# Kernel tuning notes

Measured on AMD Instinct MI355X. Metric: run time of the kernel, lower is better.

Reference implementation:

```python
import jax, jax.numpy as jnp
import numpy as np
import math

N_SLOTS, DIM, ITERS = 8, 256, 3
BATCH, TOKENS = 64, 4096


def _ln(x, g, b, eps=1e-5):
    mu = x.mean(-1, keepdims=True)
    var = ((x - mu) ** 2).mean(-1, keepdims=True)
    return (x - mu) * jax.lax.rsqrt(var + eps) * g + b


def setup_inputs() -> dict:
    key = jax.random.key(0)
    ks = jax.random.split(key, 16)
    d = DIM
    s = 0.02
    return {
        "inputs": jax.random.normal(ks[0], (BATCH, TOKENS, d), jnp.float32),
        "noise": jax.random.normal(ks[1], (BATCH, N_SLOTS, d), jnp.float32),
        "slots_mu": jax.random.normal(ks[2], (1, N_SLOTS, d), jnp.float32),
        "slots_logsigma": jnp.zeros((1, N_SLOTS, d), jnp.float32),
        "Wq": jax.random.normal(ks[3], (d, d), jnp.float32) * s,
        "Wk": jax.random.normal(ks[4], (d, d), jnp.float32) * s,
        "Wv": jax.random.normal(ks[5], (d, d), jnp.float32) * s,
        "W_ih": jax.random.normal(ks[6], (3 * d, d), jnp.float32) * s,
        "W_hh": jax.random.normal(ks[7], (3 * d, d), jnp.float32) * s,
        "b_ih": jnp.zeros((3 * d,), jnp.float32),
        "b_hh": jnp.zeros((3 * d,), jnp.float32),
        "mlp_W1": jax.random.normal(ks[8], (d, d), jnp.float32) * s,
        "mlp_b1": jnp.zeros((d,), jnp.float32),
        "mlp_W2": jax.random.normal(ks[9], (d, d), jnp.float32) * s,
        "mlp_b2": jnp.zeros((d,), jnp.float32),
        "ln_in_g": jnp.ones((d,), jnp.float32),
        "ln_in_b": jnp.zeros((d,), jnp.float32),
        "ln_slots_g": jnp.ones((d,), jnp.float32),
        "ln_slots_b": jnp.zeros((d,), jnp.float32),
        "ln_mlp_g": jnp.ones((d,), jnp.float32),
        "ln_mlp_b": jnp.zeros((d,), jnp.float32),
    }


def reference(inputs, noise, slots_mu, slots_logsigma, Wq, Wk, Wv,
              W_ih, W_hh, b_ih, b_hh, mlp_W1, mlp_b1, mlp_W2, mlp_b2,
              ln_in_g, ln_in_b, ln_slots_g, ln_slots_b, ln_mlp_g, ln_mlp_b):
    n, t, d = inputs.shape
    scale = 1.0 / math.sqrt(d)
    x = _ln(inputs, ln_in_g, ln_in_b)                      # [n,t,d]
    slots = slots_mu + jnp.exp(slots_logsigma) * noise     # [n,S,d]
    k = jnp.einsum('ntd,ed->nte', x, Wk)
    v = jnp.einsum('ntd,ed->nte', x, Wv)
    for _ in range(ITERS):
        slots_prev = slots
        q = jnp.einsum('nsd,ed->nse', _ln(slots, ln_slots_g, ln_slots_b), Wq)
        logits = jnp.einsum('nsd,ntd->nst', q, k) * scale  # [n,S,t]
        attn = jax.nn.softmax(logits, axis=-1)
        attn = attn / (attn.sum(-1, keepdims=True) + 1e-8)
        updates = jnp.einsum('nst,ntd->nsd', attn, v)      # [n,S,d]
        # GRUCell (torch gate order r,z,n)
        gi = jnp.einsum('nsd,ed->nse', updates, W_ih) + b_ih
        gh = jnp.einsum('nsd,ed->nse', slots_prev, W_hh) + b_hh
        gi_r, gi_z, gi_n = jnp.split(gi, 3, axis=-1)
        gh_r, gh_z, gh_n = jnp.split(gh, 3, axis=-1)
        r = jax.nn.sigmoid(gi_r + gh_r)
        z = jax.nn.sigmoid(gi_z + gh_z)
        h_new = jnp.tanh(gi_n + r * gh_n)
        slots = (1.0 - z) * h_new + z * slots_prev
        hid = jax.nn.relu(jnp.einsum('nsd,ed->nse', _ln(slots, ln_mlp_g, ln_mlp_b), mlp_W1) + mlp_b1)
        slots = slots + jnp.einsum('nsd,ed->nse', hid, mlp_W2) + mlp_b2
    return slots
```

## Files before the change

### kernel.cpp

```cpp
#include <hip/hip_runtime.h>
#include <math.h>

#define TOKENS 4096
#define BATCH 64

typedef __attribute__((ext_vector_type(8))) short bf16x8;
typedef __attribute__((ext_vector_type(4))) float f32x4;
union U4B { uint4 u; bf16x8 b; };
union U2x2B { uint2 u[2]; bf16x8 b; };

__device__ __forceinline__ float wsum(float v) {
#pragma unroll
  for (int m = 32; m >= 1; m >>= 1) v += __shfl_xor(v, m);
  return v;
}
__device__ __forceinline__ unsigned short f2bf(float f) {
  unsigned u = __float_as_uint(f);
  u += 0x7fffu + ((u >> 16) & 1u);
  return (unsigned short)(u >> 16);
}
__device__ __forceinline__ float bflo(unsigned p) { return __uint_as_float(p << 16); }
__device__ __forceinline__ float bfhi(unsigned p) { return __uint_as_float(p & 0xffff0000u); }
__device__ __forceinline__ float sigmf(float x) { return 1.f / (1.f + expf(-x)); }

__global__ __launch_bounds__(256) void k_pre(
    const float* __restrict__ in, const float* __restrict__ lin_g,
    const float* __restrict__ lin_b, unsigned* __restrict__ x,
    const float* __restrict__ Wq, const float* __restrict__ Wv,
    const float* __restrict__ Wih, const float* __restrict__ Whh,
    const float* __restrict__ W1, const float* __restrict__ W2,
    float* __restrict__ WqT, float* __restrict__ WvT, float* __restrict__ WihT,
    float* __restrict__ WhhT, float* __restrict__ W1T, float* __restrict__ W2T) {
  int bid = blockIdx.x, tid = threadIdx.x;
  if (bid < 65536) {
    int row = bid * 4 + (tid >> 6);
    int lane = tid & 63;
    const float* p = in + (size_t)row * 256 + lane * 4;
    float4 v = *(const float4*)p;
    float s  = wsum(v.x + v.y + v.z + v.w);
    float sq = wsum(v.x * v.x + v.y * v.y + v.z * v.z + v.w * v.w);
    float mu = s * (1.f / 256.f);
    float var = sq * (1.f / 256.f) - mu * mu;
    float rs = rsqrtf(var + 1e-5f);
    float4 gg = *(const float4*)(lin_g + lane * 4);
    float4 bb = *(const float4*)(lin_b + lane * 4);
    float y0 = (v.x - mu) * rs * gg.x + bb.x;
    float y1 = (v.y - mu) * rs * gg.y + bb.y;
    float y2 = (v.z - mu) * rs * gg.z + bb.z;
    float y3 = (v.w - mu) * rs * gg.w + bb.w;
    uint2 o;
    o.x = (unsigned)f2bf(y0) | ((unsigned)f2bf(y1) << 16);
    o.y = (unsigned)f2bf(y2) | ((unsigned)f2bf(y3) << 16);
    *(uint2*)(x + (size_t)row * 128 + lane * 2) = o;
    return;
  }
  {
    __shared__ float t[32][33];
    int t2 = bid - 65536;
    const float* S; float* D; int R; int tile;
    if (t2 < 64)       { S = Wq;  D = WqT;  R = 256; tile = t2; }
    else if (t2 < 128) { S = Wv;  D = WvT;  R = 256; tile = t2 - 64; }
    else if (t2 < 192) { S = W1;  D = W1T;  R = 256; tile = t2 - 128; }
    else if (t2 < 256) { S = W2;  D = W2T;  R = 256; tile = t2 - 192; }
    else if (t2 < 448) { S = Wih; D = WihT; R = 768; tile = t2 - 256; }
    else               { S = Whh; D = WhhT; R = 768; tile = t2 - 448; }
    int rt = R >> 5;
    int r0 = (tile % rt) * 32, c0 = (tile / rt) * 32;
    int ci = tid & 31, r8 = tid >> 5;
#pragma unroll
    for (int k = 0; k < 4; ++k) {
      int r = r8 + k * 8;
      t[r][ci] = S[(size_t)(r0 + r) * 256 + c0 + ci];
    }
    __syncthreads();
#pragma unroll
    for (int k = 0; k < 4; ++k) {
      int r = r8 + k * 8;
      D[(size_t)(c0 + r) * R + r0 + ci] = t[ci][r];
    }
  }
}

__global__ __launch_bounds__(256) void k_qw0(
    const float* __restrict__ smu, const float* __restrict__ slsig,
    const float* __restrict__ noise, const float* __restrict__ lsl_g,
    const float* __restrict__ lsl_b, const float* __restrict__ WqT,
    const float* __restrict__ Wk, float* __restrict__ slots,
    unsigned* __restrict__ qwb) {
  __shared__ float ln[256];
  __shared__ float q[256];
  __shared__ float red[8];
  int n = blockIdx.x, s = blockIdx.y, tid = threadIdx.x;
  int sd = s * 256 + tid;
  float v = smu[sd] + expf(slsig[sd]) * noise[(size_t)n * 2048 + sd];
  slots[(size_t)n * 2048 + sd] = v;
  float ps = wsum(v), pq = wsum(v * v);
  if ((tid & 63) == 0) { red[tid >> 6] = ps; red[4 + (tid >> 6)] = pq; }
  __syncthreads();
  float sum = red[0] + red[1] + red[2] + red[3];
  float sqq = red[4] + red[5] + red[6] + red[7];
  float mu = sum * (1.f / 256.f);
  float var = sqq * (1.f / 256.f) - mu * mu;
  float rs = rsqrtf(var + 1e-5f);
  ln[tid] = (v - mu) * rs * lsl_g[tid] + lsl_b[tid];
  __syncthreads();
  float a = 0.f;
  for (int d = 0; d < 256; ++d) a += ln[d] * WqT[d * 256 + tid];
  q[tid] = a;
  __syncthreads();
  float c = 0.f;
  for (int e = 0; e < 256; ++e) c += q[e] * Wk[(size_t)e * 256 + tid];
  c *= 0.0625f;
  __syncthreads();
  ln[tid] = c;
  __syncthreads();
  if (tid < 128)
    qwb[((size_t)n * 8 + s) * 128 + tid] =
        (unsigned)f2bf(ln[2 * tid]) | ((unsigned)f2bf(ln[2 * tid + 1]) << 16);
}

__global__ __launch_bounds__(256) void k_att(const unsigned* __restrict__ x,
                                             const unsigned* __restrict__ qwb,
                                             float* __restrict__ stats,
                                             float* __restrict__ axp) {
  __shared__ unsigned xs[64][130];
  __shared__ float lsT[64][8];
  __shared__ float redS[8][4];
  int ch = blockIdx.x, n = blockIdx.y;
  int tid = threadIdx.x, wv = tid >> 6, l = tid & 63;
  int col = l & 15, g = l >> 4;
  {
    int lane32 = tid & 31, g8 = tid >> 5;
    const unsigned* src = x + ((size_t)n * 4096 + ch * 64) * 128 + lane32 * 4;
#pragma unroll
    for (int p = 0; p < 8; ++p) {
      int row = p * 8 + g8;
      uint4 vv = *(const uint4*)(src + (size_t)row * 128);
      unsigned* dr = &xs[row][lane32 * 4];
      *(uint2*)dr = make_uint2(vv.x, vv.y);
      *(uint2*)(dr + 2) = make_uint2(vv.z, vv.w);
    }
  }
  uint4 a[8];
  {
    const unsigned* ap = qwb + ((size_t)n * 8 + (l & 7)) * 128 + g * 4;
#pragma unroll
    for (int kk = 0; kk < 8; ++kk) a[kk] = *(const uint4*)(ap + kk * 16);
  }
  __syncthreads();
  {
    int t0 = wv * 16;
    const unsigned* xr = &xs[t0 + col][0];
    f32x4 qacc = {0.f, 0.f, 0.f, 0.f};
#pragma unroll
    for (int kk = 0; kk < 8; ++kk) {
      U4B aa; aa.u = a[kk];
      U2x2B bb;
      bb.u[0] = *(const uint2*)(xr + kk * 16 + g * 4);
      bb.u[1] = *(const uint2*)(xr + kk * 16 + g * 4 + 2);
      qacc = __builtin_amdgcn_mfma_f32_16x16x32_bf16(aa.b, bb.b, qacc, 0, 0, 0);
    }
    if (g < 2) {
#pragma unroll
      for (int r = 0; r < 4; ++r) lsT[t0 + col][g * 4 + r] = qacc[r];
    }
  }
  __syncthreads();
  int s = tid & 7, tg = tid >> 3;
  {
    float e0 = __expf(lsT[tg][s]);
    float e1 = __expf(lsT[tg + 32][s]);
    lsT[tg][s] = e0;
    lsT[tg + 32][s] = e1;
    float S = e0 + e1;
    S += __shfl_xor(S, 8);
    S += __shfl_xor(S, 16);
    S += __shfl_xor(S, 32);
    if (l < 8) redS[s][wv] = S;
  }
  __syncthreads();
  if (tid < 8)
    stats[((size_t)n * 8 + tid) * 64 + ch] =
        redS[tid][0] + redS[tid][1] + redS[tid][2] + redS[tid][3];
  {
    int d = tid;
    float pv[8] = {0, 0, 0, 0, 0, 0, 0, 0};
#pragma unroll 8
    for (int t = 0; t < 64; ++t) {
      unsigned pw = xs[t][d >> 1];
      float xv = (d & 1) ? bfhi(pw) : bflo(pw);
      float4 p0 = *(const float4*)&lsT[t][0];
      float4 p1 = *(const float4*)&lsT[t][4];
      pv[0] += p0.x * xv; pv[1] += p0.y * xv;
      pv[2] += p0.z * xv; pv[3] += p0.w * xv;
      pv[4] += p1.x * xv; pv[5] += p1.y * xv;
      pv[6] += p1.z * xv; pv[7] += p1.w * xv;
    }
    float* op = axp + ((size_t)n * 64 + ch) * 2048 + d;
#pragma unroll
    for (int ss = 0; ss < 8; ++ss) op[ss * 256] = pv[ss];
  }
}

__global__ __launch_bounds__(512) void k_update3(
    const float* __restrict__ axp, const float* __restrict__ stats,
    const float* __restrict__ slots_in,
    const float* __restrict__ WvT, const float* __restrict__ WihT,
    const float* __restrict__ WhhT, const float* __restrict__ b_ih,
    const float* __restrict__ b_hh, const float* __restrict__ W1T,
    const float* __restrict__ b1, const float* __restrict__ W2T,
    const float* __restrict__ b2, const float* __restrict__ lml_g,
    const float* __restrict__ lml_b, const float* __restrict__ lsl_g,
    const float* __restrict__ lsl_b, const float* __restrict__ WqT,
    const float* __restrict__ Wk, unsigned* __restrict__ qwb, int doQw,
    float* __restrict__ slots_out) {
  __shared__ float ax[4][256];
  __shared__ float sp[4][256];
  __shared__ float upd[4][256];
  __shared__ float gi[4][768];
  __shared__ float gh[4][768];
  __shared__ float sn[4][256];
  __shared__ float lnv[4][256];
  __shared__ float hid[4][256];
  __shared__ float red[16];
  __shared__ float Sinv[4];
  int n = blockIdx.x, sg = blockIdx.y * 4;
  int tid = threadIdx.x;
  if (tid < 4) {
    const float* st = stats + ((size_t)n * 8 + sg + tid) * 64;
    float S = 0.f;
#pragma unroll 8
    for (int c = 0; c < 64; ++c) S += st[c];
    Sinv[tid] = 1.f / (S * (1.f + 1e-8f));
  }
  __syncthreads();
  for (int i = tid; i < 1024; i += 512) {
    int sl = i >> 8, d = i & 255;
    const float* pp = axp + (size_t)n * 131072 + (sg + sl) * 256 + d;
    float a = 0.f;
#pragma unroll 8
    for (int c = 0; c < 64; ++c) a += pp[(size_t)c * 2048];
    ax[sl][d] = a * Sinv[sl];
    sp[sl][d] = slots_in[((size_t)n * 8 + sg + sl) * 256 + d];
  }
  __syncthreads();
  int e = tid & 255, h = tid >> 8;
  {
    float a0 = 0.f, a1 = 0.f;
    for (int d = 0; d < 256; ++d) {
      float w = WvT[d * 256 + e];
      a0 += ax[h * 2][d] * w;
      a1 += ax[h * 2 + 1][d] * w;
    }
    upd[h * 2][e] = a0;
    upd[h * 2 + 1][e] = a1;
  }
  __syncthreads();
  for (int jj = tid; jj < 1536; jj += 512) {
    bool ihs = jj < 768;
    int j = ihs ? jj : jj - 768;
    const float* WT = ihs ? WihT : WhhT;
    const float* src = ihs ? &upd[0][0] : &sp[0][0];
    float a0 = 0.f, a1 = 0.f, a2 = 0.f, a3 = 0.f;
    for (int d = 0; d < 256; ++d) {
      float w = WT[(size_t)d * 768 + j];
      a0 += src[d] * w;
      a1 += src[256 + d] * w;
      a2 += src[512 + d] * w;
      a3 += src[768 + d] * w;
    }
    float bb = ihs ? b_ih[j] : b_hh[j];
    float* dst = ihs ? &gi[0][0] : &gh[0][0];
    dst[j] = a0 + bb;
    dst[768 + j] = a1 + bb;
    dst[1536 + j] = a2 + bb;
    dst[2304 + j] = a3 + bb;
  }
  __syncthreads();
  for (int i = tid; i < 1024; i += 512) {
    int sl = i >> 8, j = i & 255;
    float r = sigmf(gi[sl][j] + gh[sl][j]);
    float z = sigmf(gi[sl][j + 256] + gh[sl][j + 256]);
    float hh = tanhf(gi[sl][j + 512] + r * gh[sl][j + 512]);
    sn[sl][j] = (1.f - z) * hh + z * sp[sl][j];
  }
  __syncthreads();
  {
    int sl = tid >> 7, qq = tid & 127;
    float v0 = sn[sl][qq], v1 = sn[sl][qq + 128];
    float ps = wsum(v0 + v1);
    float pq = wsum(v0 * v0 + v1 * v1);
    int wid = tid >> 6;
    if ((tid & 63) == 0) { red[wid] = ps; red[8 + wid] = pq; }
    __syncthreads();
    float ssum = red[sl * 2] + red[sl * 2 + 1];
    float sqq  = red[8 + sl * 2] + red[8 + sl * 2 + 1];
    float mu = ssum * (1.f / 256.f);
    float var = sqq * (1.f / 256.f) - mu * mu;
    float rs = rsqrtf(var + 1e-5f);
    lnv[sl][qq]       = (v0 - mu) * rs * lml_g[qq] + lml_b[qq];
    lnv[sl][qq + 128] = (v1 - mu) * rs * lml_g[qq + 128] + lml_b[qq + 128];
  }
  __syncthreads();
  {
    float a0 = 0.f, a1 = 0.f;
    for (int d = 0; d < 256; ++d) {
      float w = W1T[d * 256 + e];
      a0 += lnv[h * 2][d] * w;
      a1 += lnv[h * 2 + 1][d] * w;
    }
    hid[h * 2][e]     = fmaxf(a0 + b1[e], 0.f);
    hid[h * 2 + 1][e] = fmaxf(a1 + b1[e], 0.f);
  }
  __syncthreads();
  {
    float a0 = 0.f, a1 = 0.f;
    for (int d = 0; d < 256; ++d) {
      float w = W2T[d * 256 + e];
      a0 += hid[h * 2][d] * w;
      a1 += hid[h * 2 + 1][d] * w;
    }
    float o0 = sn[h * 2][e] + a0 + b2[e];
    float o1 = sn[h * 2 + 1][e] + a1 + b2[e];
    slots_out[((size_t)n * 8 + sg + h * 2) * 256 + e]     = o0;
    slots_out[((size_t)n * 8 + sg + h * 2 + 1) * 256 + e] = o1;
    ax[h * 2][e] = o0;
    ax[h * 2 + 1][e] = o1;
  }
  if (!doQw) return;
  __syncthreads();
  {
    int sl = tid >> 7, qq = tid & 127;
    float v0 = ax[sl][qq], v1 = ax[sl][qq + 128];
    float ps = wsum(v0 + v1);
    float pq = wsum(v0 * v0 + v1 * v1);
    int wid = tid >> 6;
    if ((tid & 63) == 0) { red[wid] = ps; red[8 + wid] = pq; }
    __syncthreads();
    float ssum = red[sl * 2] + red[sl * 2 + 1];
    float sqq  = red[8 + sl * 2] + red[8 + sl * 2 + 1];
    float mu = ssum * (1.f / 256.f);
    float var = sqq * (1.f / 256.f) - mu * mu;
    float rs = rsqrtf(var + 1e-5f);
    sp[sl][qq]       = (v0 - mu) * rs * lsl_g[qq] + lsl_b[qq];
    sp[sl][qq + 128] = (v1 - mu) * rs * lsl_g[qq + 128] + lsl_b[qq + 128];
  }
  __syncthreads();
  {
    float a0 = 0.f, a1 = 0.f;
    for (int d = 0; d < 256; ++d) {
      float w = WqT[d * 256 + e];
      a0 += sp[h * 2][d] * w;
      a1 += sp[h * 2 + 1][d] * w;
    }
    upd[h * 2][e] = a0;
    upd[h * 2 + 1][e] = a1;
  }
  __syncthreads();
  {
    float c0 = 0.f, c1 = 0.f;
    for (int ee = 0; ee < 256; ++ee) {
      float w = Wk[(size_t)ee * 256 + e];
      c0 += upd[h * 2][ee] * w;
      c1 += upd[h * 2 + 1][ee] * w;
    }
    hid[h * 2][e]     = c0 * 0.0625f;
    hid[h * 2 + 1][e] = c1 * 0.0625f;
  }
  __syncthreads();
  {
    int sl = tid >> 7, p = tid & 127;
    qwb[((size_t)n * 8 + sg + sl) * 128 + p] =
        (unsigned)f2bf(hid[sl][2 * p]) | ((unsigned)f2bf(hid[sl][2 * p + 1]) << 16);
  }
}

extern "C" void kernel_launch(void* const* d_in, const int* in_sizes, int n_in,
                              void* d_out, int out_size, void* d_ws, size_t ws_size,
                              hipStream_t stream) {
  (void)in_sizes; (void)n_in; (void)out_size; (void)ws_size;
  const float* inputs = (const float*)d_in[0];
  const float* noise  = (const float*)d_in[1];
  const float* smu    = (const float*)d_in[2];
  const float* slsig  = (const float*)d_in[3];
  const float* Wq     = (const float*)d_in[4];
  const float* Wk     = (const float*)d_in[5];
  const float* Wv     = (const float*)d_in[6];
  const float* W_ih   = (const float*)d_in[7];
  const float* W_hh   = (const float*)d_in[8];
  const float* b_ih   = (const float*)d_in[9];
  const float* b_hh   = (const float*)d_in[10];
  const float* W1     = (const float*)d_in[11];
  const float* b1     = (const float*)d_in[12];
  const float* W2     = (const float*)d_in[13];
  const float* b2     = (const float*)d_in[14];
  const float* lin_g  = (const float*)d_in[15];
  const float* lin_b  = (const float*)d_in[16];
  const float* lsl_g  = (const float*)d_in[17];
  const float* lsl_b  = (const float*)d_in[18];
  const float* lml_g  = (const float*)d_in[19];
  const float* lml_b  = (const float*)d_in[20];
  float* out = (float*)d_out;
  char* ws = (char*)d_ws;
  unsigned* x    = (unsigned*)(ws + 0);
  unsigned* qwb  = (unsigned*)(ws + 134217728);
  float* stats   = (float*)(ws + 134479872);
  float* axp     = (float*)(ws + 134610944);
  float* WqT     = (float*)(ws + 168165376);
  float* WvT     = (float*)(ws + 168427520);
  float* WihT    = (float*)(ws + 168689664);
  float* WhhT    = (float*)(ws + 169476096);
  float* W1T     = (float*)(ws + 170262528);
  float* W2T     = (float*)(ws + 170524672);

  k_pre<<<dim3(66176), 256, 0, stream>>>(inputs, lin_g, lin_b, x,
                                         Wq, Wv, W_ih, W_hh, W1, W2,
                                         WqT, WvT, WihT, WhhT, W1T, W2T);
  k_qw0<<<dim3(BATCH, 8), 256, 0, stream>>>(smu, slsig, noise, lsl_g, lsl_b,
                                            WqT, Wk, out, qwb);
  for (int it = 0; it < 3; ++it) {
    k_att<<<dim3(64, BATCH), 256, 0, stream>>>(x, qwb, stats, axp);
    k_update3<<<dim3(BATCH, 2), 512, 0, stream>>>(
        axp, stats, out, WvT, WihT, WhhT, b_ih, b_hh, W1T, b1, W2T, b2,
        lml_g, lml_b, lsl_g, lsl_b, WqT, Wk, qwb, (it < 2) ? 1 : 0, out);
  }
}
```

Baseline: 460.8 us.

## Process two token chunks per attention block and split update kernel per slot

The attention kernel now loops over two 64-token chunks per block, accumulating the weighted-value partials and softmax sums in registers. This halves the number of partial sums written to and later reduced from global memory. The update kernel changes from 128 blocks of 512 threads handling 4 slots each to 512 blocks of 256 threads handling one slot, with the GRU gate computation fused into the matvec loop. That gives more parallel blocks for the small serial per-slot work, at the cost of rereading the weights once per slot instead of once per four slots.

```diff
diff --git a/kernel.cpp b/kernel.cpp
--- a/kernel.cpp
+++ b/kernel.cpp
@@ -119,90 +119,97 @@
         (unsigned)f2bf(ln[2 * tid]) | ((unsigned)f2bf(ln[2 * tid + 1]) << 16);
 }
 
-__global__ __launch_bounds__(256) void k_att(const unsigned* __restrict__ x,
-                                             const unsigned* __restrict__ qwb,
-                                             float* __restrict__ stats,
-                                             float* __restrict__ axp) {
+__global__ __launch_bounds__(256) void k_att2(const unsigned* __restrict__ x,
+                                              const unsigned* __restrict__ qwb,
+                                              float* __restrict__ stats,
+                                              float* __restrict__ axp) {
   __shared__ unsigned xs[64][130];
   __shared__ float lsT[64][8];
   __shared__ float redS[8][4];
-  int ch = blockIdx.x, n = blockIdx.y;
+  int bx = blockIdx.x, n = blockIdx.y;
   int tid = threadIdx.x, wv = tid >> 6, l = tid & 63;
   int col = l & 15, g = l >> 4;
-  {
-    int lane32 = tid & 31, g8 = tid >> 5;
-    const unsigned* src = x + ((size_t)n * 4096 + ch * 64) * 128 + lane32 * 4;
-#pragma unroll
-    for (int p = 0; p < 8; ++p) {
-      int row = p * 8 + g8;
-      uint4 vv = *(const uint4*)(src + (size_t)row * 128);
-      unsigned* dr = &xs[row][lane32 * 4];
-      *(uint2*)dr = make_uint2(vv.x, vv.y);
-      *(uint2*)(dr + 2) = make_uint2(vv.z, vv.w);
-    }
-  }
   uint4 a[8];
   {
     const unsigned* ap = qwb + ((size_t)n * 8 + (l & 7)) * 128 + g * 4;
 #pragma unroll
     for (int kk = 0; kk < 8; ++kk) a[kk] = *(const uint4*)(ap + kk * 16);
   }
-  __syncthreads();
-  {
-    int t0 = wv * 16;
-    const unsigned* xr = &xs[t0 + col][0];
-    f32x4 qacc = {0.f, 0.f, 0.f, 0.f};
-#pragma unroll
-    for (int kk = 0; kk < 8; ++kk) {
-      U4B aa; aa.u = a[kk];
-      U2x2B bb;
-      bb.u[0] = *(const uint2*)(xr + kk * 16 + g * 4);
-      bb.u[1] = *(const uint2*)(xr + kk * 16 + g * 4 + 2);
-      qacc = __builtin_amdgcn_mfma_f32_16x16x32_bf16(aa.b, bb.b, qacc, 0, 0, 0);
-    }
-    if (g < 2) {
-#pragma unroll
-      for (int r = 0; r < 4; ++r) lsT[t0 + col][g * 4 + r] = qacc[r];
-    }
-  }
-  __syncthreads();
+  float pv[8] = {0, 0, 0, 0, 0, 0, 0, 0};
+  float SS = 0.f;
   int s = tid & 7, tg = tid >> 3;
-  {
-    float e0 = __expf(lsT[tg][s]);
-    float e1 = __expf(lsT[tg + 32][s]);
-    lsT[tg][s] = e0;
-    lsT[tg + 32][s] = e1;
-    float S = e0 + e1;
-    S += __shfl_xor(S, 8);
-    S += __shfl_xor(S, 16);
-    S += __shfl_xor(S, 32);
-    if (l < 8) redS[s][wv] = S;
-  }
-  __syncthreads();
-  if (tid < 8)
-    stats[((size_t)n * 8 + tid) * 64 + ch] =
-        redS[tid][0] + redS[tid][1] + redS[tid][2] + redS[tid][3];
-  {
-    int d = tid;
-    float pv[8] = {0, 0, 0, 0, 0, 0, 0, 0};
+  for (int cc = 0; cc < 2; ++cc) {
+    int ch = bx * 2 + cc;
+    {
+      int lane32 = tid & 31, g8 = tid >> 5;
+      const unsigned* src = x + ((size_t)n * 4096 + ch * 64) * 128 + lane32 * 4;
+#pragma unroll
+      for (int p = 0; p < 8; ++p) {
+        int row = p * 8 + g8;
+        uint4 vv = *(const uint4*)(src + (size_t)row * 128);
+        unsigned* dr = &xs[row][lane32 * 4];
+        *(uint2*)dr = make_uint2(vv.x, vv.y);
+        *(uint2*)(dr + 2) = make_uint2(vv.z, vv.w);
+      }
+    }
+    __syncthreads();
+    {
+      int t0 = wv * 16;
+      const unsigned* xr = &xs[t0 + col][0];
+      f32x4 qacc = {0.f, 0.f, 0.f, 0.f};
+#pragma unroll
+      for (int kk = 0; kk < 8; ++kk) {
+        U4B aa; aa.u = a[kk];
+        U2x2B bb;
+        bb.u[0] = *(const uint2*)(xr + kk * 16 + g * 4);
+        bb.u[1] = *(const uint2*)(xr + kk * 16 + g * 4 + 2);
+        qacc = __builtin_amdgcn_mfma_f32_16x16x32_bf16(aa.b, bb.b, qacc, 0, 0, 0);
+      }
+      if (g < 2) {
+#pragma unroll
+        for (int r = 0; r < 4; ++r) lsT[t0 + col][g * 4 + r] = qacc[r];
+      }
+    }
+    __syncthreads();
+    {
+      float e0 = __expf(lsT[tg][s]);
+      float e1 = __expf(lsT[tg + 32][s]);
+      lsT[tg][s] = e0;
+      lsT[tg + 32][s] = e1;
+      float S = e0 + e1;
+      S += __shfl_xor(S, 8);
+      S += __shfl_xor(S, 16);
+      S += __shfl_xor(S, 32);
+      if (l < 8) redS[s][wv] = S;
+    }
+    __syncthreads();
+    if (tid < 8)
+      SS += redS[tid][0] + redS[tid][1] + redS[tid][2] + redS[tid][3];
+    {
+      int d = tid;
 #pragma unroll 8
-    for (int t = 0; t < 64; ++t) {
-      unsigned pw = xs[t][d >> 1];
-      float xv = (d & 1) ? bfhi(pw) : bflo(pw);
-      float4 p0 = *(const float4*)&lsT[t][0];
-      float4 p1 = *(const float4*)&lsT[t][4];
-      pv[0] += p0.x * xv; pv[1] += p0.y * xv;
-      pv[2] += p0.z * xv; pv[3] += p0.w * xv;
-      pv[4] += p1.x * xv; pv[5] += p1.y * xv;
-      pv[6] += p1.z * xv; pv[7] += p1.w * xv;
-    }
-    float* op = axp + ((size_t)n * 64 + ch) * 2048 + d;
+      for (int t = 0; t < 64; ++t) {
+        unsigned pw = xs[t][d >> 1];
+        float xv = (d & 1) ? bfhi(pw) : bflo(pw);
+        float4 p0 = *(const float4*)&lsT[t][0];
+        float4 p1 = *(const float4*)&lsT[t][4];
+        pv[0] += p0.x * xv; pv[1] += p0.y * xv;
+        pv[2] += p0.z * xv; pv[3] += p0.w * xv;
+        pv[4] += p1.x * xv; pv[5] += p1.y * xv;
+        pv[6] += p1.z * xv; pv[7] += p1.w * xv;
+      }
+    }
+    __syncthreads();
+  }
+  if (tid < 8) stats[((size_t)n * 8 + tid) * 32 + bx] = SS;
+  {
+    float* op = axp + ((size_t)n * 32 + bx) * 2048 + tid;
 #pragma unroll
     for (int ss = 0; ss < 8; ++ss) op[ss * 256] = pv[ss];
   }
 }
 
-__global__ __launch_bounds__(512) void k_update3(
+__global__ __launch_bounds__(256) void k_update5(
     const float* __restrict__ axp, const float* __restrict__ stats,
     const float* __restrict__ slots_in,
     const float* __restrict__ WvT, const float* __restrict__ WihT,
@@ -214,165 +221,112 @@
     const float* __restrict__ lsl_b, const float* __restrict__ WqT,
     const float* __restrict__ Wk, unsigned* __restrict__ qwb, int doQw,
     float* __restrict__ slots_out) {
-  __shared__ float ax[4][256];
-  __shared__ float sp[4][256];
-  __shared__ float upd[4][256];
-  __shared__ float gi[4][768];
-  __shared__ float gh[4][768];
-  __shared__ float sn[4][256];
-  __shared__ float lnv[4][256];
-  __shared__ float hid[4][256];
-  __shared__ float red[16];
-  __shared__ float Sinv[4];
-  int n = blockIdx.x, sg = blockIdx.y * 4;
-  int tid = threadIdx.x;
-  if (tid < 4) {
-    const float* st = stats + ((size_t)n * 8 + sg + tid) * 64;
-    float S = 0.f;
+  __shared__ float ax[256];
+  __shared__ float sp[256];
+  __shared__ float upd[256];
+  __shared__ float sn[256];
+  __shared__ float lnv[256];
+  __shared__ float hid[256];
+  __shared__ float red[8];
+  int n = blockIdx.x, s = blockIdx.y, tid = threadIdx.x;
+  {
+    float sv = 0.f;
+    if (tid < 32) sv = stats[((size_t)n * 8 + s) * 32 + tid];
+    if (tid < 64) {
+      sv = wsum(sv);
+      if (tid == 0) red[0] = 1.f / (sv * (1.f + 1e-8f));
+    }
+  }
+  {
+    const float* pp = axp + (size_t)n * 65536 + s * 256 + tid;
+    float acc = 0.f;
 #pragma unroll 8
-    for (int c = 0; c < 64; ++c) S += st[c];
-    Sinv[tid] = 1.f / (S * (1.f + 1e-8f));
-  }
-  __syncthreads();
-  for (int i = tid; i < 1024; i += 512) {
-    int sl = i >> 8, d = i & 255;
-    const float* pp = axp + (size_t)n * 131072 + (sg + sl) * 256 + d;
-    float a = 0.f;
-#pragma unroll 8
-    for (int c = 0; c < 64; ++c) a += pp[(size_t)c * 2048];
-    ax[sl][d] = a * Sinv[sl];
-    sp[sl][d] = slots_in[((size_t)n * 8 + sg + sl) * 256 + d];
-  }
-  __syncthreads();
-  int e = tid & 255, h = tid >> 8;
-  {
-    float a0 = 0.f, a1 = 0.f;
+    for (int c = 0; c < 32; ++c) acc += pp[(size_t)c * 2048];
+    sp[tid] = slots_in[((size_t)n * 8 + s) * 256 + tid];
+    __syncthreads();
+    ax[tid] = acc * red[0];
+  }
+  __syncthreads();
+  {
+    float a0 = 0.f;
+    for (int d = 0; d < 256; ++d) a0 += ax[d] * WvT[d * 256 + tid];
+    upd[tid] = a0;
+  }
+  __syncthreads();
+  {
+    int j = tid;
+    float gr = 0.f, gz = 0.f, gn = 0.f, hr = 0.f, hz = 0.f, hn = 0.f;
     for (int d = 0; d < 256; ++d) {
-      float w = WvT[d * 256 + e];
-      a0 += ax[h * 2][d] * w;
-      a1 += ax[h * 2 + 1][d] * w;
-    }
-    upd[h * 2][e] = a0;
-    upd[h * 2 + 1][e] = a1;
-  }
-  __syncthreads();
-  for (int jj = tid; jj < 1536; jj += 512) {
-    bool ihs = jj < 768;
-    int j = ihs ? jj : jj - 768;
-    const float* WT = ihs ? WihT : WhhT;
-    const float* src = ihs ? &upd[0][0] : &sp[0][0];
-    float a0 = 0.f, a1 = 0.f, a2 = 0.f, a3 = 0.f;
-    for (int d = 0; d < 256; ++d) {
-      float w = WT[(size_t)d * 768 + j];
-      a0 += src[d] * w;
-      a1 += src[256 + d] * w;
-      a2 += src[512 + d] * w;
-      a3 += src[768 + d] * w;
-    }
-    float bb = ihs ? b_ih[j] : b_hh[j];
-    float* dst = ihs ? &gi[0][0] : &gh[0][0];
-    dst[j] = a0 + bb;
-    dst[768 + j] = a1 + bb;
-    dst[1536 + j] = a2 + bb;
-    dst[2304 + j] = a3 + bb;
-  }
-  __syncthreads();
-  for (int i = tid; i < 1024; i += 512) {
-    int sl = i >> 8, j = i & 255;
-    float r = sigmf(gi[sl][j] + gh[sl][j]);
-    float z = sigmf(gi[sl][j + 256] + gh[sl][j + 256]);
-    float hh = tanhf(gi[sl][j + 512] + r * gh[sl][j + 512]);
-    sn[sl][j] = (1.f - z) * hh + z * sp[sl][j];
-  }
-  __syncthreads();
-  {
-    int sl = tid >> 7, qq = tid & 127;
-    float v0 = sn[sl][qq], v1 = sn[sl][qq + 128];
-    float ps = wsum(v0 + v1);
-    float pq = wsum(v0 * v0 + v1 * v1);
-    int wid = tid >> 6;
-    if ((tid & 63) == 0) { red[wid] = ps; red[8 + wid] = pq; }
-    __syncthreads();
-    float ssum = red[sl * 2] + red[sl * 2 + 1];
-    float sqq  = red[8 + sl * 2] + red[8 + sl * 2 + 1];
-    float mu = ssum * (1.f / 256.f);
+      float u = upd[d], s_ = sp[d];
+      gr += u * WihT[d * 768 + j];
+      gz += u * WihT[d * 768 + j + 256];
+      gn += u * WihT[d * 768 + j + 512];
+      hr += s_ * WhhT[d * 768 + j];
+      hz += s_ * WhhT[d * 768 + j + 256];
+      hn += s_ * WhhT[d * 768 + j + 512];
+    }
+    float r = sigmf(gr + b_ih[j] + hr + b_hh[j]);
+    float z = sigmf(gz + b_ih[j + 256] + hz + b_hh[j + 256]);
+    float hh = tanhf(gn + b_ih[j + 512] + r * (hn + b_hh[j + 512]));
+    sn[j] = (1.f - z) * hh + z * sp[j];
+  }
+  __syncthreads();
+  {
+    float v = sn[tid];
+    float ps = wsum(v), pq = wsum(v * v);
+    if ((tid & 63) == 0) { red[tid >> 6] = ps; red[4 + (tid >> 6)] = pq; }
+    __syncthreads();
+    float sum = red[0] + red[1] + red[2] + red[3];
+    float sqq = red[4] + red[5] + red[6] + red[7];
+    float mu = sum * (1.f / 256.f);
     float var = sqq * (1.f / 256.f) - mu * mu;
     float rs = rsqrtf(var + 1e-5f);
-    lnv[sl][qq]       = (v0 - mu) * rs * lml_g[qq] + lml_b[qq];
-    lnv[sl][qq + 128] = (v1 - mu) * rs * lml_g[qq + 128] + lml_b[qq + 128];
-  }
-  __syncthreads();
-  {
-    float a0 = 0.f, a1 = 0.f;
-    for (int d = 0; d < 256; ++d) {
-      float w = W1T[d * 256 + e];
-      a0 += lnv[h * 2][d] * w;
-      a1 += lnv[h * 2 + 1][d] * w;
-    }
-    hid[h * 2][e]     = fmaxf(a0 + b1[e], 0.f);
-    hid[h * 2 + 1][e] = fmaxf(a1 + b1[e], 0.f);
-  }
-  __syncthreads();
-  {
-    float a0 = 0.f, a1 = 0.f;
-    for (int d = 0; d < 256; ++d) {
-      float w = W2T[d * 256 + e];
-      a0 += hid[h * 2][d] * w;
-      a1 += hid[h * 2 + 1][d] * w;
-    }
-    float o0 = sn[h * 2][e] + a0 + b2[e];
-    float o1 = sn[h * 2 + 1][e] + a1 + b2[e];
-    slots_out[((size_t)n * 8 + sg + h * 2) * 256 + e]     = o0;
-    slots_out[((size_t)n * 8 + sg + h * 2 + 1) * 256 + e] = o1;
-    ax[h * 2][e] = o0;
-    ax[h * 2 + 1][e] = o1;
+    lnv[tid] = (v - mu) * rs * lml_g[tid] + lml_b[tid];
+  }
+  __syncthreads();
+  {
+    float a0 = 0.f;
+    for (int d = 0; d < 256; ++d) a0 += lnv[d] * W1T[d * 256 + tid];
+    hid[tid] = fmaxf(a0 + b1[tid], 0.f);
+  }
+  __syncthreads();
+  {
+    float a0 = 0.f;
+    for (int d = 0; d < 256; ++d) a0 += hid[d] * W2T[d * 256 + tid];
+    float o = sn[tid] + a0 + b2[tid];
+    slots_out[((size_t)n * 8 + s) * 256 + tid] = o;
+    ax[tid] = o;
   }
   if (!doQw) return;
   __syncthreads();
   {
-    int sl = tid >> 7, qq = tid & 127;
-    float v0 = ax[sl][qq], v1 = ax[sl][qq + 128];
-    float ps = wsum(v0 + v1);
-    float pq = wsum(v0 * v0 + v1 * v1);
-    int wid = tid >> 6;
-    if ((tid & 63) == 0) { red[wid] = ps; red[8 + wid] = pq; }
-    __syncthreads();
-    float ssum = red[sl * 2] + red[sl * 2 + 1];
-    float sqq  = red[8 + sl * 2] + red[8 + sl * 2 + 1];
-    float mu = ssum * (1.f / 256.f);
+    float v = ax[tid];
+    float ps = wsum(v), pq = wsum(v * v);
+    if ((tid & 63) == 0) { red[tid >> 6] = ps; red[4 + (tid >> 6)] = pq; }
+    __syncthreads();
+    float sum = red[0] + red[1] + red[2] + red[3];
+    float sqq = red[4] + red[5] + red[6] + red[7];
+    float mu = sum * (1.f / 256.f);
     float var = sqq * (1.f / 256.f) - mu * mu;
     float rs = rsqrtf(var + 1e-5f);
-    sp[sl][qq]       = (v0 - mu) * rs * lsl_g[qq] + lsl_b[qq];
-    sp[sl][qq + 128] = (v1 - mu) * rs * lsl_g[qq + 128] + lsl_b[qq + 128];
-  }
-  __syncthreads();
-  {
-    float a0 = 0.f, a1 = 0.f;
-    for (int d = 0; d < 256; ++d) {
-      float w = WqT[d * 256 + e];
-      a0 += sp[h * 2][d] * w;
-      a1 += sp[h * 2 + 1][d] * w;
-    }
-    upd[h * 2][e] = a0;
-    upd[h * 2 + 1][e] = a1;
-  }
-  __syncthreads();
-  {
-    float c0 = 0.f, c1 = 0.f;
-    for (int ee = 0; ee < 256; ++ee) {
-      float w = Wk[(size_t)ee * 256 + e];
-      c0 += upd[h * 2][ee] * w;
-      c1 += upd[h * 2 + 1][ee] * w;
-    }
-    hid[h * 2][e]     = c0 * 0.0625f;
-    hid[h * 2 + 1][e] = c1 * 0.0625f;
-  }
-  __syncthreads();
-  {
-    int sl = tid >> 7, p = tid & 127;
-    qwb[((size_t)n * 8 + sg + sl) * 128 + p] =
-        (unsigned)f2bf(hid[sl][2 * p]) | ((unsigned)f2bf(hid[sl][2 * p + 1]) << 16);
-  }
+    sp[tid] = (v - mu) * rs * lsl_g[tid] + lsl_b[tid];
+  }
+  __syncthreads();
+  {
+    float a0 = 0.f;
+    for (int d = 0; d < 256; ++d) a0 += sp[d] * WqT[d * 256 + tid];
+    upd[tid] = a0;
+  }
+  __syncthreads();
+  {
+    float c0 = 0.f;
+    for (int ee = 0; ee < 256; ++ee) c0 += upd[ee] * Wk[(size_t)ee * 256 + tid];
+    hid[tid] = c0 * 0.0625f;
+  }
+  __syncthreads();
+  if (tid < 128)
+    qwb[((size_t)n * 8 + s) * 128 + tid] =
+        (unsigned)f2bf(hid[2 * tid]) | ((unsigned)f2bf(hid[2 * tid + 1]) << 16);
 }
 
 extern "C" void kernel_launch(void* const* d_in, const int* in_sizes, int n_in,
@@ -419,8 +373,8 @@
   k_qw0<<<dim3(BATCH, 8), 256, 0, stream>>>(smu, slsig, noise, lsl_g, lsl_b,
                                             WqT, Wk, out, qwb);
   for (int it = 0; it < 3; ++it) {
-    k_att<<<dim3(64, BATCH), 256, 0, stream>>>(x, qwb, stats, axp);
-    k_update3<<<dim3(BATCH, 2), 512, 0, stream>>>(
+    k_att2<<<dim3(32, BATCH), 256, 0, stream>>>(x, qwb, stats, axp);
+    k_update5<<<dim3(BATCH, 8), 256, 0, stream>>>(
         axp, stats, out, WvT, WihT, WhhT, b_ih, b_hh, W1T, b1, W2T, b2,
         lml_g, lml_b, lsl_g, lsl_b, WqT, Wk, qwb, (it < 2) ? 1 : 0, out);
   }
```

Result: faster. 388.7 us (-15.7%).
